# Kernel optimization log

Measured on AMD Instinct MI355X. Metric: run time of the kernel, lower is better.

Reference implementation:

```python
import jax, jax.numpy as jnp
import numpy as np

H = 2048
MAX_DEPTH = 2
BASIS = 4


def setup_inputs() -> dict:
    key = jax.random.key(0)
    ks = jax.random.split(key, 16)
    s = 0.02

    def w(k, shape):
        return jax.random.normal(k, shape, dtype=jnp.float32) * s

    return dict(
        x=jax.random.normal(ks[0], (1, H), dtype=jnp.float32),
        h=jax.random.normal(ks[1], (1, H), dtype=jnp.float32),
        c=jax.random.normal(ks[2], (1, H), dtype=jnp.float32),
        Wq=w(ks[3], (H, H)), Wk=w(ks[4], (H, H)), Wv=w(ks[5], (H, H)), Wo=w(ks[6], (H, H)),
        Wih=w(ks[7], (H, 4 * H)), Whh=w(ks[8], (H, 4 * H)),
        b_lstm=jnp.zeros((4 * H,), jnp.float32),
        router_w=w(ks[9], (H, BASIS)), router_b=jnp.zeros((BASIS,), jnp.float32),
        expert_w=w(ks[10], (BASIS, H, H)), expert_b=jnp.zeros((BASIS, H), jnp.float32),
        dr_w=w(ks[11], (H, MAX_DEPTH + 1)),
        # bias the depth router toward the deepest choice so the recursion tree is exercised
        dr_b=jnp.array([0.0, 1.0, 5.0], jnp.float32),
        ram_w=w(ks[12], (2 * H, H)), ram_b=jnp.zeros((H,), jnp.float32),
        ag_w=w(ks[13], (2 * H, H)), ag_b=jnp.zeros((H,), jnp.float32),
    )


def reference(x, h, c, Wq, Wk, Wv, Wo, Wih, Whh, b_lstm, router_w, router_b,
              expert_w, expert_b, dr_w, dr_b, ram_w, ram_b, ag_w, ag_b):
    def cell_step(x_, h_, c_):
        # Single-token multi-head attention: softmax over a length-1 axis is
        # identically 1, so attention collapses to (h @ Wv) @ Wo; Wq/Wk are
        # parameters with zero effective gradient (matches torch behavior).
        attn = (h_ @ Wv) @ Wo
        gates = x_ @ Wih + attn @ Whh + b_lstm  # [1, 4H]
        i, f, g, o = jnp.split(gates, 4, axis=1)
        c2 = jax.nn.sigmoid(f) * c_ + jax.nn.sigmoid(i) * jnp.tanh(g)
        h2 = jax.nn.sigmoid(o) * jnp.tanh(c2)
        return h2, h2, c2

    def path_gate(hh):
        p = jax.nn.softmax(hh @ router_w + router_b, axis=1)          # [1, E]
        eo = jnp.einsum('bh,ehk->bek', hh, expert_w) + expert_b        # [1, E, H]
        return jnp.einsum('be,bek->bk', p, eo)                         # [1, H]

    def ramanujan(states):
        # alternating-harmonic (Ramanujan-summation style) weighted reduction
        agg = states[0] * 0.0
        for n, s in enumerate(states):
            agg = agg + (((-1.0) ** n) / (n + 1)) * s
        return jnp.concatenate([agg, states[0]], axis=1) @ ram_w + ram_b

    def fwd(x_, h_, c_, depth):
        so, hs, cs = cell_step(x_, h_, c_)
        hp = path_gate(hs)
        # mirrors torch.no_grad() + .item() host sync
        chosen = int(jnp.argmax(hp @ dr_w + dr_b, axis=1)[0])
        steps = min(chosen, max(0, MAX_DEPTH - depth))
        if steps <= 0:
            return so, hp, cs
        h_cur, c_cur, final = hp, cs, so
        states = [h_cur]
        for _ in range(steps):
            damping = 1.0 / (depth + 1) ** 2
            ro, hnr, cn = fwd(x_, h_cur, c_cur, depth + 1)
            h_next = h_cur + damping * (hnr - h_cur)  # torch.lerp
            states.append(h_next)
            h_cur, c_cur, final = h_next, cn, ro
        anchor = ramanujan(states)
        g = jax.nn.sigmoid(jnp.concatenate([h_cur, anchor], axis=1) @ ag_w + ag_b)
        return final, g * anchor + (1.0 - g) * h_cur, c_cur

    return fwd(x, h, c, 0)
```

## Files before the change

### kernel.cpp

```cpp
#include <hip/hip_runtime.h>
#include <math.h>


#define H 2048

struct P {
  const float *x, *h0, *c0, *Wv, *Wo, *Wih, *Whh, *b_lstm, *router_w, *router_b,
              *expert_w, *expert_b, *dr_w, *dr_b, *ram_w, *ram_b, *ag_w, *ag_b;
  float* out;
  float* ws;
};

constexpr int CTRU   = 2304;
constexpr int DL     = 2304;
constexpr int GT     = 2320;
constexpr int NODE   = 10512;
constexpr int NODESZ = 26624;
constexpr int THV = 0, ATT = 2048, GAC = 4096, EO = 12288, SO = 20480, CS = 22528, HP = 24576;
constexpr int FIN    = NODE + 5 * NODESZ;
constexpr int FINSZ  = 8192;
constexpr int ANC = 0, GCC = 2048, HNo = 4096, AGGo = 6144;
constexpr int RH1 = FIN + 3 * FINSZ;
constexpr int RF1 = RH1 + 2048;
constexpr int RC1 = RH1 + 4096;

__device__ __forceinline__ float sigm(float v) { return 1.f / (1.f + expf(-v)); }

__device__ __forceinline__ float coh_f(const float* p) {
  return __hip_atomic_load(p, __ATOMIC_RELAXED, __HIP_MEMORY_SCOPE_AGENT);
}
__device__ __forceinline__ void coh_st(float* p, float v) {
  __hip_atomic_store(p, v, __ATOMIC_RELAXED, __HIP_MEMORY_SCOPE_AGENT);
}

__device__ __forceinline__ int dsteps(const float* dla, const float* drb, int mx) {
  const float l0 = dla[0] + drb[0], l1 = dla[1] + drb[1], l2 = dla[2] + drb[2];
  int ch = 0; float bv = l0;
  if (l1 > bv) { bv = l1; ch = 1; }
  if (l2 > bv) { bv = l2; ch = 2; }
  return ch < mx ? ch : mx;
}

__device__ __forceinline__ bool pred(const float* ws, const float* drb, int code) {
  if (code == 0) return true;
  const int s0 = dsteps(ws + DL, drb, 2);
  switch (code) {
    case 1: return s0 >= 1;
    case 2: return s0 >= 1 && dsteps(ws + DL + 4, drb, 1) >= 1;
    case 3: return s0 >= 2;
    case 4: return s0 >= 2 && dsteps(ws + DL + 8, drb, 1) >= 1;
  }
  return true;
}

__device__ __forceinline__ void resbar(unsigned* ctr, int phase) {
  asm volatile("s_waitcnt vmcnt(0)" ::: "memory");
  __syncthreads();
  if (threadIdx.x == 0) {
    unsigned* sub = ctr + (blockIdx.x & 7) * 16;
    unsigned* master = ctr + 128;
    const unsigned prev = __hip_atomic_fetch_add(sub, 1u, __ATOMIC_RELAXED, __HIP_MEMORY_SCOPE_AGENT);
    if (prev == (unsigned)(64 * phase) - 1u)
      __hip_atomic_fetch_add(master, 1u, __ATOMIC_RELAXED, __HIP_MEMORY_SCOPE_AGENT);
    long t = 0;
    while (__hip_atomic_load(master, __ATOMIC_RELAXED, __HIP_MEMORY_SCOPE_AGENT) <
           (unsigned)(8 * phase)) {
      __builtin_amdgcn_s_sleep(8);
      if (++t > 20000000L) break;
    }
  }
  __syncthreads();
}

__device__ __forceinline__ void gemv_phase(
    int bid, int G, int chunk,
    const float* xA, const float* xB, int splitPt, const float* xBias, int xmode,
    const float* __restrict__ W, float* __restrict__ y, int N,
    float* shx, float4* red)
{
  const int tid = threadIdx.x, lane = tid & 63, tsub = tid >> 6;
  const int g = bid % G, s = bid / G;
  const int base = s * chunk;
  for (int idx = tid; idx < chunk; idx += 256) {
    const int i = base + idx;
    float v;
    if (xmode == 0)      v = (i < splitPt) ? xA[i] : xB[i - splitPt];
    else if (xmode == 1) v = coh_f(xA + i);
    else                 v = (i < splitPt) ? xA[i] : (xBias[i - splitPt] + coh_f(xB + (i - splitPt)));
    shx[idx] = v;
  }
  __syncthreads();
  const int len = chunk >> 2;
  const int j = (g << 8) + (lane << 2);
  const float* Wp = W + (size_t)(base + tsub * len) * N + j;
  float ax = 0.f, ay = 0.f, az = 0.f, aw = 0.f;
  for (int t = 0; t < len; ++t) {
    const float xi = shx[tsub * len + t];
    const float4 wv = *reinterpret_cast<const float4*>(Wp);
    ax = fmaf(xi, wv.x, ax); ay = fmaf(xi, wv.y, ay);
    az = fmaf(xi, wv.z, az); aw = fmaf(xi, wv.w, aw);
    Wp += N;
  }
  red[tid] = make_float4(ax, ay, az, aw);
  __syncthreads();
  if (tsub == 0) {
    float4 a = red[tid], b = red[tid + 64], c = red[tid + 128], d = red[tid + 192];
    atomicAdd(&y[j + 0], a.x + b.x + c.x + d.x);
    atomicAdd(&y[j + 1], a.y + b.y + c.y + d.y);
    atomicAdd(&y[j + 2], a.z + b.z + c.z + d.z);
    atomicAdd(&y[j + 3], a.w + b.w + c.w + d.w);
  }
}

__device__ void expert_phase(const P& p, float* nb, const float* c_in, const float* gt,
                             float* shx, float4* red)
{
  const int tid = threadIdx.x, lane = tid & 63, w = tid >> 6;
  const int g = blockIdx.x & 31, s = blockIdx.x >> 5;
  const int i0 = s * 128;
  if (tid < 128) {
    const int i = i0 + tid;
    const float gi = p.b_lstm[i]         + coh_f(gt + i)         + coh_f(nb + GAC + i);
    const float gf = p.b_lstm[H + i]     + coh_f(gt + H + i)     + coh_f(nb + GAC + H + i);
    const float gg = p.b_lstm[2 * H + i] + coh_f(gt + 2 * H + i) + coh_f(nb + GAC + 2 * H + i);
    const float go = p.b_lstm[3 * H + i] + coh_f(gt + 3 * H + i) + coh_f(nb + GAC + 3 * H + i);
    const float c2 = sigm(gf) * c_in[i] + sigm(gi) * tanhf(gg);
    const float h2 = sigm(go) * tanhf(c2);
    shx[tid] = h2;
    if (g == 0) { coh_st(nb + SO + i, h2); coh_st(nb + CS + i, c2); }
  }
  __syncthreads();
  const int j = (g << 8) + (lane << 2);
  const int e = j >> 11, k = j & (H - 1);
  const float* Wp = p.expert_w + ((size_t)e << 22) + (size_t)(i0 + w * 32) * H + k;
  float ax = 0.f, ay = 0.f, az = 0.f, aw = 0.f;
  for (int t = 0; t < 32; ++t) {
    const float xi = shx[w * 32 + t];
    const float4 wv = *reinterpret_cast<const float4*>(Wp);
    ax = fmaf(xi, wv.x, ax); ay = fmaf(xi, wv.y, ay);
    az = fmaf(xi, wv.z, az); aw = fmaf(xi, wv.w, aw);
    Wp += H;
  }
  red[tid] = make_float4(ax, ay, az, aw);
  __syncthreads();
  if (w == 0) {
    float4 a = red[tid], b = red[tid + 64], c = red[tid + 128], d = red[tid + 192];
    atomicAdd(&nb[EO + j + 0], a.x + b.x + c.x + d.x);
    atomicAdd(&nb[EO + j + 1], a.y + b.y + c.y + d.y);
    atomicAdd(&nb[EO + j + 2], a.z + b.z + c.z + d.z);
    atomicAdd(&nb[EO + j + 3], a.w + b.w + c.w + d.w);
  }
}

__device__ void combine_phase(const P& p, float* nb, float* dla, int leaf, float damping,
                              const float* php, float* hn, float* agg, float4* red)
{
  const int tid = threadIdx.x;
  float r0 = 0.f, r1 = 0.f, r2 = 0.f, r3 = 0.f;
  for (int i = tid; i < H; i += 256) {
    const float hh = coh_f(nb + SO + i);
    const float4 rw = *reinterpret_cast<const float4*>(p.router_w + i * 4);
    r0 = fmaf(hh, rw.x, r0); r1 = fmaf(hh, rw.y, r1);
    r2 = fmaf(hh, rw.z, r2); r3 = fmaf(hh, rw.w, r3);
  }
  red[tid] = make_float4(r0, r1, r2, r3);
  __syncthreads();
  for (int off = 128; off > 0; off >>= 1) {
    if (tid < off) {
      const float4 b = red[tid + off];
      red[tid].x += b.x; red[tid].y += b.y; red[tid].z += b.z; red[tid].w += b.w;
    }
    __syncthreads();
  }
  const float4 L = red[0];
  __syncthreads();
  const float l0 = L.x + p.router_b[0], l1 = L.y + p.router_b[1];
  const float l2 = L.z + p.router_b[2], l3 = L.w + p.router_b[3];
  const float m = fmaxf(fmaxf(l0, l1), fmaxf(l2, l3));
  const float e0 = expf(l0 - m), e1 = expf(l1 - m), e2 = expf(l2 - m), e3 = expf(l3 - m);
  const float inv = 1.f / (e0 + e1 + e2 + e3);
  const float q0 = e0 * inv, q1 = e1 * inv, q2 = e2 * inv, q3 = e3 * inv;
  const int jj = blockIdx.x * 256 + tid;
  const float v = q0 * (p.expert_b[jj]         + coh_f(nb + EO + jj))
                + q1 * (p.expert_b[H + jj]     + coh_f(nb + EO + H + jj))
                + q2 * (p.expert_b[2 * H + jj] + coh_f(nb + EO + 2 * H + jj))
                + q3 * (p.expert_b[3 * H + jj] + coh_f(nb + EO + 3 * H + jj));
  if (leaf) {
    const float h0v = php[jj];
    const float hnv = h0v + damping * (v - h0v);
    hn[jj] = hnv;
    agg[jj] = h0v - 0.5f * hnv;
  } else {
    nb[HP + jj] = v;
    red[tid] = make_float4(v * p.dr_w[jj * 3 + 0], v * p.dr_w[jj * 3 + 1], v * p.dr_w[jj * 3 + 2], 0.f);
    __syncthreads();
    for (int off = 128; off > 0; off >>= 1) {
      if (tid < off) {
        const float4 b = red[tid + off];
        red[tid].x += b.x; red[tid].y += b.y; red[tid].z += b.z;
      }
      __syncthreads();
    }
    if (tid == 0) {
      atomicAdd(&dla[0], red[0].x);
      atomicAdd(&dla[1], red[0].y);
      atomicAdd(&dla[2], red[0].z);
    }
  }
}

__device__ void tail_fsel(const P& p, float* ws) {
  if (dsteps(ws + DL, p.dr_b, 2) < 1) return;
  const bool deep = dsteps(ws + DL + 4, p.dr_b, 1) >= 1;
  const int jj = blockIdx.x * 256 + threadIdx.x;
  const float* n1 = ws + NODE + 1 * NODESZ;
  const float* n2 = ws + NODE + 2 * NODESZ;
  const float* fb = ws + FIN;
  float rh, rf, rc;
  if (deep) {
    const float gacc = p.ag_b[jj] + coh_f(fb + GCC + jj);
    const float anc  = p.ram_b[jj] + coh_f(fb + ANC + jj);
    const float hnv  = fb[HNo + jj];
    const float g = sigm(gacc);
    rh = g * anc + (1.f - g) * hnv;
    rf = n2[SO + jj]; rc = n2[CS + jj];
  } else {
    rh = n1[HP + jj]; rf = n1[SO + jj]; rc = n1[CS + jj];
  }
  ws[RH1 + jj] = rh; ws[RF1 + jj] = rf; ws[RC1 + jj] = rc;
}

__device__ void tail1(const P& p, float* ws) {
  const int s0 = dsteps(ws + DL, p.dr_b, 2);
  if (s0 < 1) return;
  const int jj = blockIdx.x * 256 + threadIdx.x;
  const float* n0 = ws + NODE;
  const float* n3 = ws + NODE + 3 * NODESZ;
  const float* n4 = ws + NODE + 4 * NODESZ;
  const float* fb3 = ws + FIN + FINSZ;
  float* fb0 = ws + FIN + 2 * FINSZ;
  const float r1 = ws[RH1 + jj];
  float rh3 = 0.f, rf3 = 0.f, rc3 = 0.f;
  if (s0 >= 2) {
    if (dsteps(ws + DL + 8, p.dr_b, 1) >= 1) {
      const float gacc = p.ag_b[jj] + coh_f(fb3 + GCC + jj);
      const float anc  = p.ram_b[jj] + coh_f(fb3 + ANC + jj);
      const float hnv  = fb3[HNo + jj];
      const float g = sigm(gacc);
      rh3 = g * anc + (1.f - g) * hnv;
      rf3 = n4[SO + jj]; rc3 = n4[CS + jj];
    } else { rh3 = n3[HP + jj]; rf3 = n3[SO + jj]; rc3 = n3[CS + jj]; }
  }
  float ag = n0[HP + jj] - 0.5f * r1;
  float hc, oF, oC;
  if (s0 >= 2) { ag += (1.f / 3.f) * rh3; hc = rh3; oF = rf3; oC = rc3; }
  else { hc = r1; oF = ws[RF1 + jj]; oC = ws[RC1 + jj]; }
  fb0[AGGo + jj] = ag; fb0[HNo + jj] = hc;
  p.out[jj] = oF; p.out[2 * H + jj] = oC;
}

__device__ void tail2(const P& p, float* ws) {
  const int s0 = dsteps(ws + DL, p.dr_b, 2);
  const int jj = blockIdx.x * 256 + threadIdx.x;
  const float* n0 = ws + NODE;
  const float* fb0 = ws + FIN + 2 * FINSZ;
  if (s0 == 0) {
    p.out[jj] = n0[SO + jj]; p.out[H + jj] = n0[HP + jj]; p.out[2 * H + jj] = n0[CS + jj];
  } else {
    const float gacc = p.ag_b[jj] + coh_f(fb0 + GCC + jj);
    const float anc  = p.ram_b[jj] + coh_f(fb0 + ANC + jj);
    const float hc   = fb0[HNo + jj];
    const float g = sigm(gacc);
    p.out[H + jj] = g * anc + (1.f - g) * hc;
  }
}

__global__ void __launch_bounds__(256, 2) k_init(P p) {
  float* ws = p.ws;
  const int gtid = blockIdx.x * 256 + threadIdx.x;
  const int gsz = 512 * 256;
  unsigned* u = (unsigned*)ws;
  for (int i = gtid; i < CTRU; i += gsz) u[i] = 0u;
  for (int i = gtid; i < 12; i += gsz) ws[DL + i] = 0.f;
  for (int i = gtid; i < 8192; i += gsz) ws[GT + i] = 0.f;
  for (int n = 0; n < 5; ++n) {
    float* nb = ws + NODE + n * NODESZ;
    for (int i = gtid; i < 20480; i += gsz) nb[i] = 0.f;
  }
  for (int q = 0; q < 3; ++q) {
    float* fb = ws + FIN + q * FINSZ;
    for (int i = gtid; i < 4096; i += gsz) fb[i] = 0.f;
  }
}

__global__ void __launch_bounds__(256, 2) k_node(
    P p, int nodeIdx, int ctrIdx, int predCode,
    const float* hv, const float* cv,
    int leaf, float damping, const float* php, float* hn, float* agg,
    float* dla, int withWih)
{
  float* ws = p.ws;
  if (!pred(ws, p.dr_b, predCode)) return;
  __shared__ float shx[256];
  __shared__ float4 red[256];
  float* nb = ws + NODE + nodeIdx * NODESZ;
  unsigned* ctr = (unsigned*)ws + ctrIdx * 256;
  if (withWih) {
    if (blockIdx.x < 256)
      gemv_phase(blockIdx.x, 8, 64, hv, hv, 1 << 30, nullptr, 0, p.Wv, nb + THV, H, shx, red);
    else
      gemv_phase(blockIdx.x - 256, 32, 256, p.x, p.x, 1 << 30, nullptr, 0, p.Wih, ws + GT, 4 * H, shx, red);
  } else {
    gemv_phase(blockIdx.x, 8, 32, hv, hv, 1 << 30, nullptr, 0, p.Wv, nb + THV, H, shx, red);
  }
  resbar(ctr, 1);
  gemv_phase(blockIdx.x, 8, 32, nb + THV, nullptr, 0, nullptr, 1, p.Wo, nb + ATT, H, shx, red);
  resbar(ctr, 2);
  gemv_phase(blockIdx.x, 32, 128, nb + ATT, nullptr, 0, nullptr, 1, p.Whh, nb + GAC, 4 * H, shx, red);
  resbar(ctr, 3);
  expert_phase(p, nb, cv, ws + GT, shx, red);
  resbar(ctr, 4);
  if (blockIdx.x >= 8) return;
  combine_phase(p, nb, dla, leaf, damping, php, hn, agg, red);
}

__global__ void __launch_bounds__(256, 2) k_fin(
    P p, int finIdx, int ctrIdx, int predCode,
    const float* aggv, const float* phpv, const float* hnv, int tailKind)
{
  float* ws = p.ws;
  __shared__ float shx[256];
  __shared__ float4 red[256];
  float* fb = ws + FIN + finIdx * FINSZ;
  unsigned* ctr = (unsigned*)ws + ctrIdx * 256;
  const bool ok = pred(ws, p.dr_b, predCode);
  if (ok) {
    gemv_phase(blockIdx.x, 8, 64, aggv, phpv, H, nullptr, 0, p.ram_w, fb + ANC, H, shx, red);
    resbar(ctr, 1);
    gemv_phase(blockIdx.x, 8, 64, hnv, fb + ANC, H, p.ram_b, 2, p.ag_w, fb + GCC, H, shx, red);
    resbar(ctr, 2);
  }
  if (blockIdx.x >= 8) return;
  if (tailKind == 1) tail_fsel(p, ws);
  else if (tailKind == 2) tail1(p, ws);
  else tail2(p, ws);
}

extern "C" void kernel_launch(void* const* d_in, const int* in_sizes, int n_in,
                              void* d_out, int out_size, void* d_ws, size_t ws_size,
                              hipStream_t stream) {
  P p;
  p.x = (const float*)d_in[0];  p.h0 = (const float*)d_in[1];  p.c0 = (const float*)d_in[2];
  p.Wv = (const float*)d_in[5]; p.Wo = (const float*)d_in[6];
  p.Wih = (const float*)d_in[7]; p.Whh = (const float*)d_in[8];
  p.b_lstm = (const float*)d_in[9];
  p.router_w = (const float*)d_in[10]; p.router_b = (const float*)d_in[11];
  p.expert_w = (const float*)d_in[12]; p.expert_b = (const float*)d_in[13];
  p.dr_w = (const float*)d_in[14]; p.dr_b = (const float*)d_in[15];
  p.ram_w = (const float*)d_in[16]; p.ram_b = (const float*)d_in[17];
  p.ag_w = (const float*)d_in[18]; p.ag_b = (const float*)d_in[19];
  p.out = (float*)d_out;
  p.ws = (float*)d_ws;

  float* ws = p.ws;
  auto nb = [&](int n) { return ws + NODE + n * NODESZ; };
  float* fb1 = ws + FIN;
  float* fb3 = ws + FIN + FINSZ;
  float* fb0 = ws + FIN + 2 * FINSZ;

  k_init<<<512, 256, 0, stream>>>(p);
  k_node<<<512, 256, 0, stream>>>(p, 0, 0, 0, p.h0, p.c0,
                                  0, 0.f, nullptr, nullptr, nullptr, ws + DL, 1);
  k_node<<<512, 256, 0, stream>>>(p, 1, 1, 1, nb(0) + HP, nb(0) + CS,
                                  0, 0.f, nullptr, nullptr, nullptr, ws + DL + 4, 0);
  k_node<<<512, 256, 0, stream>>>(p, 2, 2, 2, nb(1) + HP, nb(1) + CS,
                                  1, 0.25f, nb(1) + HP, fb1 + HNo, fb1 + AGGo, nullptr, 0);
  k_fin<<<512, 256, 0, stream>>>(p, 0, 3, 2, fb1 + AGGo, nb(1) + HP, fb1 + HNo, 1);
  k_node<<<512, 256, 0, stream>>>(p, 3, 4, 3, ws + RH1, ws + RC1,
                                  0, 0.f, nullptr, nullptr, nullptr, ws + DL + 8, 0);
  k_node<<<512, 256, 0, stream>>>(p, 4, 5, 4, nb(3) + HP, nb(3) + CS,
                                  1, 0.25f, nb(3) + HP, fb3 + HNo, fb3 + AGGo, nullptr, 0);
  k_fin<<<512, 256, 0, stream>>>(p, 1, 6, 4, fb3 + AGGo, nb(3) + HP, fb3 + HNo, 2);
  k_fin<<<512, 256, 0, stream>>>(p, 2, 7, 1, fb0 + AGGo, nb(0) + HP, fb0 + HNo, 3);
}
```

Measured before the change: 380.7 us.

## Double grid size, template gemv chunks, split Wih GEMV into its own kernel

Grid size goes from 512 to 1024 blocks per kernel, and the per-block chunk sizes are halved. The software grid barrier grows to 16 sub-counters with a shorter sleep. gemv_phase is templated on chunk size and input mode so its inner loops fully unroll. The x@Wih GEMV and the node/fin workspace zeroing move out of the first node kernel into a separate k_wih kernel, leaving a small k_zero for counters. The aim is more memory-level parallelism for the bandwidth-bound GEMVs, at the cost of one more launch, more atomics per output, and a barrier that only works if all 1024 blocks are co-resident (occupancy 4 per CU).

```diff
diff --git a/kernel.cpp b/kernel.cpp
--- a/kernel.cpp
+++ b/kernel.cpp
@@ -3,6 +3,7 @@
 
 
 #define H 2048
+#define NB 1024
 
 struct P {
   const float *x, *h0, *c0, *Wv, *Wo, *Wih, *Whh, *b_lstm, *router_w, *router_b,
@@ -11,10 +12,10 @@
   float* ws;
 };
 
-constexpr int CTRU   = 2304;
-constexpr int DL     = 2304;
-constexpr int GT     = 2320;
-constexpr int NODE   = 10512;
+constexpr int CTRU   = 4096;
+constexpr int DL     = 4096;
+constexpr int GT     = 4112;
+constexpr int NODE   = 12304;
 constexpr int NODESZ = 26624;
 constexpr int THV = 0, ATT = 2048, GAC = 4096, EO = 12288, SO = 20480, CS = 22528, HP = 24576;
 constexpr int FIN    = NODE + 5 * NODESZ;
@@ -23,6 +24,7 @@
 constexpr int RH1 = FIN + 3 * FINSZ;
 constexpr int RF1 = RH1 + 2048;
 constexpr int RC1 = RH1 + 4096;
+constexpr int ZTOT = 5 * 20480 + 3 * 4096;
 
 __device__ __forceinline__ float sigm(float v) { return 1.f / (1.f + expf(-v)); }
 
@@ -57,49 +59,50 @@
   asm volatile("s_waitcnt vmcnt(0)" ::: "memory");
   __syncthreads();
   if (threadIdx.x == 0) {
-    unsigned* sub = ctr + (blockIdx.x & 7) * 16;
-    unsigned* master = ctr + 128;
+    unsigned* sub = ctr + (blockIdx.x & 15) * 16;
+    unsigned* master = ctr + 256;
     const unsigned prev = __hip_atomic_fetch_add(sub, 1u, __ATOMIC_RELAXED, __HIP_MEMORY_SCOPE_AGENT);
     if (prev == (unsigned)(64 * phase) - 1u)
       __hip_atomic_fetch_add(master, 1u, __ATOMIC_RELAXED, __HIP_MEMORY_SCOPE_AGENT);
     long t = 0;
     while (__hip_atomic_load(master, __ATOMIC_RELAXED, __HIP_MEMORY_SCOPE_AGENT) <
-           (unsigned)(8 * phase)) {
-      __builtin_amdgcn_s_sleep(8);
-      if (++t > 20000000L) break;
-    }
-  }
-  __syncthreads();
-}
-
+           (unsigned)(16 * phase)) {
+      __builtin_amdgcn_s_sleep(4);
+      if (++t > 50000000L) break;
+    }
+  }
+  __syncthreads();
+}
+
+template <int CHUNK, int XMODE>
 __device__ __forceinline__ void gemv_phase(
-    int bid, int G, int chunk,
-    const float* xA, const float* xB, int splitPt, const float* xBias, int xmode,
+    int bid, int G,
+    const float* xA, const float* xB, int splitPt, const float* xBias,
     const float* __restrict__ W, float* __restrict__ y, int N,
     float* shx, float4* red)
 {
   const int tid = threadIdx.x, lane = tid & 63, tsub = tid >> 6;
   const int g = bid % G, s = bid / G;
-  const int base = s * chunk;
-  for (int idx = tid; idx < chunk; idx += 256) {
+  const int base = s * CHUNK;
+  for (int idx = tid; idx < CHUNK; idx += 256) {
     const int i = base + idx;
     float v;
-    if (xmode == 0)      v = (i < splitPt) ? xA[i] : xB[i - splitPt];
-    else if (xmode == 1) v = coh_f(xA + i);
+    if (XMODE == 0)      v = (i < splitPt) ? xA[i] : xB[i - splitPt];
+    else if (XMODE == 1) v = coh_f(xA + i);
     else                 v = (i < splitPt) ? xA[i] : (xBias[i - splitPt] + coh_f(xB + (i - splitPt)));
     shx[idx] = v;
   }
   __syncthreads();
-  const int len = chunk >> 2;
+  constexpr int LEN = CHUNK / 4;
   const int j = (g << 8) + (lane << 2);
-  const float* Wp = W + (size_t)(base + tsub * len) * N + j;
+  const float* Wp = W + (size_t)(base + tsub * LEN) * N + j;
   float ax = 0.f, ay = 0.f, az = 0.f, aw = 0.f;
-  for (int t = 0; t < len; ++t) {
-    const float xi = shx[tsub * len + t];
-    const float4 wv = *reinterpret_cast<const float4*>(Wp);
+#pragma unroll
+  for (int t = 0; t < LEN; ++t) {
+    const float xi = shx[tsub * LEN + t];
+    const float4 wv = *reinterpret_cast<const float4*>(Wp + (size_t)t * N);
     ax = fmaf(xi, wv.x, ax); ay = fmaf(xi, wv.y, ay);
     az = fmaf(xi, wv.z, az); aw = fmaf(xi, wv.w, aw);
-    Wp += N;
   }
   red[tid] = make_float4(ax, ay, az, aw);
   __syncthreads();
@@ -117,8 +120,8 @@
 {
   const int tid = threadIdx.x, lane = tid & 63, w = tid >> 6;
   const int g = blockIdx.x & 31, s = blockIdx.x >> 5;
-  const int i0 = s * 128;
-  if (tid < 128) {
+  const int i0 = s * 64;
+  if (tid < 64) {
     const int i = i0 + tid;
     const float gi = p.b_lstm[i]         + coh_f(gt + i)         + coh_f(nb + GAC + i);
     const float gf = p.b_lstm[H + i]     + coh_f(gt + H + i)     + coh_f(nb + GAC + H + i);
@@ -132,14 +135,14 @@
   __syncthreads();
   const int j = (g << 8) + (lane << 2);
   const int e = j >> 11, k = j & (H - 1);
-  const float* Wp = p.expert_w + ((size_t)e << 22) + (size_t)(i0 + w * 32) * H + k;
+  const float* Wp = p.expert_w + ((size_t)e << 22) + (size_t)(i0 + w * 16) * H + k;
   float ax = 0.f, ay = 0.f, az = 0.f, aw = 0.f;
-  for (int t = 0; t < 32; ++t) {
-    const float xi = shx[w * 32 + t];
-    const float4 wv = *reinterpret_cast<const float4*>(Wp);
+#pragma unroll
+  for (int t = 0; t < 16; ++t) {
+    const float xi = shx[w * 16 + t];
+    const float4 wv = *reinterpret_cast<const float4*>(Wp + (size_t)t * H);
     ax = fmaf(xi, wv.x, ax); ay = fmaf(xi, wv.y, ay);
     az = fmaf(xi, wv.z, az); aw = fmaf(xi, wv.w, aw);
-    Wp += H;
   }
   red[tid] = make_float4(ax, ay, az, aw);
   __syncthreads();
@@ -220,9 +223,8 @@
   if (deep) {
     const float gacc = p.ag_b[jj] + coh_f(fb + GCC + jj);
     const float anc  = p.ram_b[jj] + coh_f(fb + ANC + jj);
-    const float hnv  = fb[HNo + jj];
     const float g = sigm(gacc);
-    rh = g * anc + (1.f - g) * hnv;
+    rh = g * anc + (1.f - g) * fb[HNo + jj];
     rf = n2[SO + jj]; rc = n2[CS + jj];
   } else {
     rh = n1[HP + jj]; rf = n1[SO + jj]; rc = n1[CS + jj];
@@ -245,9 +247,8 @@
     if (dsteps(ws + DL + 8, p.dr_b, 1) >= 1) {
       const float gacc = p.ag_b[jj] + coh_f(fb3 + GCC + jj);
       const float anc  = p.ram_b[jj] + coh_f(fb3 + ANC + jj);
-      const float hnv  = fb3[HNo + jj];
       const float g = sigm(gacc);
-      rh3 = g * anc + (1.f - g) * hnv;
+      rh3 = g * anc + (1.f - g) * fb3[HNo + jj];
       rf3 = n4[SO + jj]; rc3 = n4[CS + jj];
     } else { rh3 = n3[HP + jj]; rf3 = n3[SO + jj]; rc3 = n3[CS + jj]; }
   }
@@ -269,54 +270,54 @@
   } else {
     const float gacc = p.ag_b[jj] + coh_f(fb0 + GCC + jj);
     const float anc  = p.ram_b[jj] + coh_f(fb0 + ANC + jj);
-    const float hc   = fb0[HNo + jj];
     const float g = sigm(gacc);
-    p.out[H + jj] = g * anc + (1.f - g) * hc;
-  }
-}
-
-__global__ void __launch_bounds__(256, 2) k_init(P p) {
+    p.out[H + jj] = g * anc + (1.f - g) * fb0[HNo + jj];
+  }
+}
+
+__global__ void __launch_bounds__(256) k_zero(P p) {
   float* ws = p.ws;
   const int gtid = blockIdx.x * 256 + threadIdx.x;
-  const int gsz = 512 * 256;
+  const int gsz = gridDim.x * 256;
   unsigned* u = (unsigned*)ws;
   for (int i = gtid; i < CTRU; i += gsz) u[i] = 0u;
-  for (int i = gtid; i < 12; i += gsz) ws[DL + i] = 0.f;
+  if (gtid < 12) ws[DL + gtid] = 0.f;
   for (int i = gtid; i < 8192; i += gsz) ws[GT + i] = 0.f;
-  for (int n = 0; n < 5; ++n) {
-    float* nb = ws + NODE + n * NODESZ;
-    for (int i = gtid; i < 20480; i += gsz) nb[i] = 0.f;
-  }
-  for (int q = 0; q < 3; ++q) {
-    float* fb = ws + FIN + q * FINSZ;
-    for (int i = gtid; i < 4096; i += gsz) fb[i] = 0.f;
-  }
-}
-
-__global__ void __launch_bounds__(256, 2) k_node(
+}
+
+__global__ void __launch_bounds__(256, 4) k_wih(P p) {
+  float* ws = p.ws;
+  __shared__ float shx[64];
+  __shared__ float4 red[256];
+  const int gtid = blockIdx.x * 256 + threadIdx.x;
+  for (int i = gtid; i < ZTOT; i += NB * 256) {
+    if (i < 5 * 20480) {
+      const int n = i / 20480, off = i % 20480;
+      ws[NODE + n * NODESZ + off] = 0.f;
+    } else {
+      const int j = i - 5 * 20480;
+      ws[FIN + (j >> 12) * FINSZ + (j & 4095)] = 0.f;
+    }
+  }
+  gemv_phase<64, 0>(blockIdx.x, 32, p.x, p.x, 1 << 30, nullptr, p.Wih, ws + GT, 4 * H, shx, red);
+}
+
+__global__ void __launch_bounds__(256, 4) k_node(
     P p, int nodeIdx, int ctrIdx, int predCode,
     const float* hv, const float* cv,
-    int leaf, float damping, const float* php, float* hn, float* agg,
-    float* dla, int withWih)
+    int leaf, float damping, const float* php, float* hn, float* agg, float* dla)
 {
   float* ws = p.ws;
   if (!pred(ws, p.dr_b, predCode)) return;
-  __shared__ float shx[256];
+  __shared__ float shx[64];
   __shared__ float4 red[256];
   float* nb = ws + NODE + nodeIdx * NODESZ;
-  unsigned* ctr = (unsigned*)ws + ctrIdx * 256;
-  if (withWih) {
-    if (blockIdx.x < 256)
-      gemv_phase(blockIdx.x, 8, 64, hv, hv, 1 << 30, nullptr, 0, p.Wv, nb + THV, H, shx, red);
-    else
-      gemv_phase(blockIdx.x - 256, 32, 256, p.x, p.x, 1 << 30, nullptr, 0, p.Wih, ws + GT, 4 * H, shx, red);
-  } else {
-    gemv_phase(blockIdx.x, 8, 32, hv, hv, 1 << 30, nullptr, 0, p.Wv, nb + THV, H, shx, red);
-  }
+  unsigned* ctr = (unsigned*)ws + ctrIdx * 512;
+  gemv_phase<16, 0>(blockIdx.x, 8, hv, hv, 1 << 30, nullptr, p.Wv, nb + THV, H, shx, red);
   resbar(ctr, 1);
-  gemv_phase(blockIdx.x, 8, 32, nb + THV, nullptr, 0, nullptr, 1, p.Wo, nb + ATT, H, shx, red);
+  gemv_phase<16, 1>(blockIdx.x, 8, nb + THV, nullptr, 0, nullptr, p.Wo, nb + ATT, H, shx, red);
   resbar(ctr, 2);
-  gemv_phase(blockIdx.x, 32, 128, nb + ATT, nullptr, 0, nullptr, 1, p.Whh, nb + GAC, 4 * H, shx, red);
+  gemv_phase<64, 1>(blockIdx.x, 32, nb + ATT, nullptr, 0, nullptr, p.Whh, nb + GAC, 4 * H, shx, red);
   resbar(ctr, 3);
   expert_phase(p, nb, cv, ws + GT, shx, red);
   resbar(ctr, 4);
@@ -324,20 +325,20 @@
   combine_phase(p, nb, dla, leaf, damping, php, hn, agg, red);
 }
 
-__global__ void __launch_bounds__(256, 2) k_fin(
+__global__ void __launch_bounds__(256, 4) k_fin(
     P p, int finIdx, int ctrIdx, int predCode,
     const float* aggv, const float* phpv, const float* hnv, int tailKind)
 {
   float* ws = p.ws;
-  __shared__ float shx[256];
+  __shared__ float shx[64];
   __shared__ float4 red[256];
   float* fb = ws + FIN + finIdx * FINSZ;
-  unsigned* ctr = (unsigned*)ws + ctrIdx * 256;
+  unsigned* ctr = (unsigned*)ws + ctrIdx * 512;
   const bool ok = pred(ws, p.dr_b, predCode);
   if (ok) {
-    gemv_phase(blockIdx.x, 8, 64, aggv, phpv, H, nullptr, 0, p.ram_w, fb + ANC, H, shx, red);
+    gemv_phase<32, 0>(blockIdx.x, 8, aggv, phpv, H, nullptr, p.ram_w, fb + ANC, H, shx, red);
     resbar(ctr, 1);
-    gemv_phase(blockIdx.x, 8, 64, hnv, fb + ANC, H, p.ram_b, 2, p.ag_w, fb + GCC, H, shx, red);
+    gemv_phase<32, 2>(blockIdx.x, 8, hnv, fb + ANC, H, p.ram_b, p.ag_w, fb + GCC, H, shx, red);
     resbar(ctr, 2);
   }
   if (blockIdx.x >= 8) return;
@@ -368,18 +369,19 @@
   float* fb3 = ws + FIN + FINSZ;
   float* fb0 = ws + FIN + 2 * FINSZ;
 
-  k_init<<<512, 256, 0, stream>>>(p);
-  k_node<<<512, 256, 0, stream>>>(p, 0, 0, 0, p.h0, p.c0,
-                                  0, 0.f, nullptr, nullptr, nullptr, ws + DL, 1);
-  k_node<<<512, 256, 0, stream>>>(p, 1, 1, 1, nb(0) + HP, nb(0) + CS,
-                                  0, 0.f, nullptr, nullptr, nullptr, ws + DL + 4, 0);
-  k_node<<<512, 256, 0, stream>>>(p, 2, 2, 2, nb(1) + HP, nb(1) + CS,
-                                  1, 0.25f, nb(1) + HP, fb1 + HNo, fb1 + AGGo, nullptr, 0);
-  k_fin<<<512, 256, 0, stream>>>(p, 0, 3, 2, fb1 + AGGo, nb(1) + HP, fb1 + HNo, 1);
-  k_node<<<512, 256, 0, stream>>>(p, 3, 4, 3, ws + RH1, ws + RC1,
-                                  0, 0.f, nullptr, nullptr, nullptr, ws + DL + 8, 0);
-  k_node<<<512, 256, 0, stream>>>(p, 4, 5, 4, nb(3) + HP, nb(3) + CS,
-                                  1, 0.25f, nb(3) + HP, fb3 + HNo, fb3 + AGGo, nullptr, 0);
-  k_fin<<<512, 256, 0, stream>>>(p, 1, 6, 4, fb3 + AGGo, nb(3) + HP, fb3 + HNo, 2);
-  k_fin<<<512, 256, 0, stream>>>(p, 2, 7, 1, fb0 + AGGo, nb(0) + HP, fb0 + HNo, 3);
-}
+  k_zero<<<32, 256, 0, stream>>>(p);
+  k_wih<<<NB, 256, 0, stream>>>(p);
+  k_node<<<NB, 256, 0, stream>>>(p, 0, 0, 0, p.h0, p.c0,
+                                 0, 0.f, nullptr, nullptr, nullptr, ws + DL);
+  k_node<<<NB, 256, 0, stream>>>(p, 1, 1, 1, nb(0) + HP, nb(0) + CS,
+                                 0, 0.f, nullptr, nullptr, nullptr, ws + DL + 4);
+  k_node<<<NB, 256, 0, stream>>>(p, 2, 2, 2, nb(1) + HP, nb(1) + CS,
+                                 1, 0.25f, nb(1) + HP, fb1 + HNo, fb1 + AGGo, nullptr);
+  k_fin<<<NB, 256, 0, stream>>>(p, 0, 3, 2, fb1 + AGGo, nb(1) + HP, fb1 + HNo, 1);
+  k_node<<<NB, 256, 0, stream>>>(p, 3, 4, 3, ws + RH1, ws + RC1,
+                                 0, 0.f, nullptr, nullptr, nullptr, ws + DL + 8);
+  k_node<<<NB, 256, 0, stream>>>(p, 4, 5, 4, nb(3) + HP, nb(3) + CS,
+                                 1, 0.25f, nb(3) + HP, fb3 + HNo, fb3 + AGGo, nullptr);
+  k_fin<<<NB, 256, 0, stream>>>(p, 1, 6, 4, fb3 + AGGo, nb(3) + HP, fb3 + HNo, 2);
+  k_fin<<<NB, 256, 0, stream>>>(p, 2, 7, 1, fb0 + AGGo, nb(0) + HP, fb0 + HNo, 3);
+}
```

New measurement: 501.2 us. +31.7%, slower.
